# Kernel optimization log

Measured on AMD Instinct MI355X. Metric: run time of the kernel, lower is better.

Reference implementation:

```python
import jax, jax.numpy as jnp
import numpy as np

N, E, D = 50000, 600000, 128


def gcn_conv(x, edge_index, edge_weight, W, b, num_nodes):
    # PyG GCNConv (add_self_loops=False): out = D^{-1/2} A D^{-1/2} (x W) + b
    row, col = edge_index[0], edge_index[1]  # source, target
    deg = jax.ops.segment_sum(edge_weight, col, num_segments=num_nodes)  # [N]
    dis = jnp.where(deg > 0, jax.lax.rsqrt(jnp.where(deg > 0, deg, 1.0)), 0.0)
    norm = dis[row] * edge_weight * dis[col]  # [E]
    xl = x @ W  # [N, out]
    msg = xl[row] * norm[:, None]  # [E, out] gather + scale
    out = jax.ops.segment_sum(msg, col, num_segments=num_nodes)  # scatter-add
    return out + b


def setup_inputs() -> dict:
    key = jax.random.key(0)
    ks = jax.random.split(key, 7)
    x = jax.random.normal(ks[0], (N, D), dtype=jnp.float32)
    adj = jax.random.randint(ks[1], (2, E), 0, N, dtype=jnp.int64)
    edge_weights = jax.random.uniform(ks[2], (E,), dtype=jnp.float32)
    s = 1.0 / np.sqrt(D)
    W1 = jax.random.uniform(ks[3], (D, D), jnp.float32, -s, s)
    b1 = jnp.zeros((D,), jnp.float32)
    W2 = jax.random.uniform(ks[4], (D, D), jnp.float32, -s, s)
    b2 = jnp.zeros((D,), jnp.float32)
    return {"x": x, "adj": adj, "edge_weights": edge_weights,
            "W1": W1, "b1": b1, "W2": W2, "b2": b2}


def reference(x, adj, edge_weights, W1, b1, W2, b2):
    res = x
    h = gcn_conv(x, adj, edge_weights, W1, b1, N)
    h = jax.nn.relu(h)  # dropout is identity in eval mode
    h = gcn_conv(h, adj, edge_weights, W2, b2, N)
    h = jax.nn.relu(h)
    return h + res
```

## Files before the change

kernel.cpp:

```cpp
#include <hip/hip_runtime.h>
#include <hip/hip_bf16.h>

#define FEAT 128
#define CAP 64

typedef __attribute__((ext_vector_type(8))) short bf16x8;
typedef __attribute__((ext_vector_type(4))) float f32x4;

__device__ __forceinline__ short f2bf(float f) {
    __hip_bfloat16 h = __float2bfloat16(f);
    return *reinterpret_cast<short*>(&h);
}

__global__ __launch_bounds__(256) void k_prep(const float* __restrict__ W1,
                                              const float* __restrict__ W2,
                                              unsigned short* __restrict__ WT1,
                                              unsigned short* __restrict__ WT2,
                                              int* __restrict__ cur, int Nn) {
    const int tid = blockIdx.x * 256 + threadIdx.x;
    if (tid < FEAT * FEAT) {
        const int k = tid >> 7, n = tid & 127;
        WT1[n * FEAT + k] = (unsigned short)f2bf(W1[tid]);
        WT2[n * FEAT + k] = (unsigned short)f2bf(W2[tid]);
    }
    if (tid < Nn) cur[tid] = 0;
}

template <bool BF16IN>
__device__ __forceinline__ void gemm_tile(const void* __restrict__ Xv,
                                          const unsigned short* __restrict__ WT,
                                          unsigned short* __restrict__ Y,
                                          int Nn, int blk, int t) {
    const int rowBase = blk * 64;
    const int w = t >> 6;
    const int lane = t & 63;
    const int m = lane & 15;
    const int quad = lane >> 4;
    const int ar = rowBase + w * 16 + m;

    f32x4 acc[8] = {};
#pragma unroll
    for (int ks = 0; ks < 4; ++ks) {
        const int k0 = ks * 32 + quad * 8;
        bf16x8 a = {0, 0, 0, 0, 0, 0, 0, 0};
        if (ar < Nn) {
            if (BF16IN) {
                a = *(const bf16x8*)((const unsigned short*)Xv + (size_t)ar * FEAT + k0);
            } else {
                const float* xp = (const float*)Xv + (size_t)ar * FEAT + k0;
                const float4 v0 = *(const float4*)xp;
                const float4 v1 = *(const float4*)(xp + 4);
                a[0] = f2bf(v0.x); a[1] = f2bf(v0.y); a[2] = f2bf(v0.z); a[3] = f2bf(v0.w);
                a[4] = f2bf(v1.x); a[5] = f2bf(v1.y); a[6] = f2bf(v1.z); a[7] = f2bf(v1.w);
            }
        }
#pragma unroll
        for (int nt = 0; nt < 8; ++nt) {
            bf16x8 b = *(const bf16x8*)(WT + (size_t)(nt * 16 + m) * FEAT + k0);
            acc[nt] = __builtin_amdgcn_mfma_f32_16x16x32_bf16(a, b, acc[nt], 0, 0, 0);
        }
    }

#pragma unroll
    for (int nt = 0; nt < 8; ++nt) {
#pragma unroll
        for (int r4 = 0; r4 < 4; ++r4) {
            int gr = rowBase + w * 16 + quad * 4 + r4;
            if (gr < Nn)
                Y[(size_t)gr * FEAT + nt * 16 + m] = (unsigned short)f2bf(acc[nt][r4]);
        }
    }
}

__device__ __forceinline__ void fill_body(const int* __restrict__ row,
                                          const int* __restrict__ col,
                                          const float* __restrict__ ew,
                                          int* __restrict__ cur,
                                          unsigned long long* __restrict__ bucket,
                                          int E, int blk, int t) {
    int e = blk * 256 + t;
    if (e >= E) return;
    int c = col[e];
    int slot = atomicAdd(&cur[c], 1);
    if (slot < CAP) {
        unsigned long long v = (unsigned long long)(unsigned int)row[e] |
                               ((unsigned long long)__float_as_uint(ew[e]) << 32);
        bucket[(size_t)c * CAP + slot] = v;
    }
}

__global__ __launch_bounds__(256) void k_fused_gemm1_fill(
        const float* __restrict__ x, const unsigned short* __restrict__ WT1,
        unsigned short* __restrict__ xl, int Nn,
        const int* __restrict__ row, const int* __restrict__ col,
        const float* __restrict__ ew, int* __restrict__ cur,
        unsigned long long* __restrict__ bucket, int E, int gG) {
    if ((int)blockIdx.x < gG)
        gemm_tile<false>((const void*)x, WT1, xl, Nn, blockIdx.x, threadIdx.x);
    else
        fill_body(row, col, ew, cur, bucket, E, blockIdx.x - gG, threadIdx.x);
}

__global__ __launch_bounds__(256) void k_gemm2(const unsigned short* __restrict__ h1b,
                                               const unsigned short* __restrict__ WT2,
                                               unsigned short* __restrict__ xl, int Nn) {
    gemm_tile<true>((const void*)h1b, WT2, xl, Nn, blockIdx.x, threadIdx.x);
}

__global__ __launch_bounds__(256) void k_deg_dis(const int* __restrict__ cur,
                                                 const unsigned long long* __restrict__ bucket,
                                                 float* __restrict__ dis, int Nn) {
    const int n = (blockIdx.x * 256 + threadIdx.x) >> 6;
    const int lane = threadIdx.x & 63;
    if (n >= Nn) return;
    const int cnt = min(cur[n], CAP);
    float v = 0.0f;
    if (lane < cnt) {
        unsigned long long b = bucket[(size_t)n * CAP + lane];
        v = __uint_as_float((unsigned int)(b >> 32));
    }
#pragma unroll
    for (int m = 1; m < 64; m <<= 1) v += __shfl_xor(v, m, 64);
    if (lane == 0) dis[n] = (v > 0.0f) ? rsqrtf(v) : 0.0f;
}

template <int MODE>
__global__ __launch_bounds__(256) void k_gather(const int* __restrict__ cur,
                                                const unsigned long long* __restrict__ bucket,
                                                const float* __restrict__ dis,
                                                const unsigned int* __restrict__ XL2,
                                                const float* __restrict__ bias,
                                                const float* __restrict__ xres,
                                                void* __restrict__ OUTv, int Nn) {
    const int n = (blockIdx.x * 256 + threadIdx.x) >> 6;
    const int lane = threadIdx.x & 63;
    if (n >= Nn) return;
    const int cnt = min(cur[n], CAP);
    const float dn = dis[n];

    const uint2 be = ((const uint2*)(bucket + (size_t)n * CAP))[lane];
    const int   srcv = (int)be.x;
    float wv = 0.0f;
    if (lane < cnt) wv = __uint_as_float(be.y) * dis[be.x];

    float ax = 0.0f, ay = 0.0f;
    int e = 0;
    for (; e + 8 <= cnt; e += 8) {
        int s[8];
        float w[8];
        unsigned int p[8];
#pragma unroll
        for (int j = 0; j < 8; ++j) {
            s[j] = __shfl(srcv, e + j, 64);
            w[j] = __shfl(wv, e + j, 64);
        }
#pragma unroll
        for (int j = 0; j < 8; ++j) p[j] = XL2[(size_t)s[j] * (FEAT / 2) + lane];
#pragma unroll
        for (int j = 0; j < 8; ++j) {
            ax += __uint_as_float(p[j] << 16) * w[j];
            ay += __uint_as_float(p[j] & 0xffff0000u) * w[j];
        }
    }
    for (; e + 4 <= cnt; e += 4) {
        int s[4];
        float w[4];
        unsigned int p[4];
#pragma unroll
        for (int j = 0; j < 4; ++j) {
            s[j] = __shfl(srcv, e + j, 64);
            w[j] = __shfl(wv, e + j, 64);
        }
#pragma unroll
        for (int j = 0; j < 4; ++j) p[j] = XL2[(size_t)s[j] * (FEAT / 2) + lane];
#pragma unroll
        for (int j = 0; j < 4; ++j) {
            ax += __uint_as_float(p[j] << 16) * w[j];
            ay += __uint_as_float(p[j] & 0xffff0000u) * w[j];
        }
    }
    for (; e < cnt; ++e) {
        const int s = __shfl(srcv, e, 64);
        const float w = __shfl(wv, e, 64);
        const unsigned int p = XL2[(size_t)s * (FEAT / 2) + lane];
        ax += __uint_as_float(p << 16) * w;
        ay += __uint_as_float(p & 0xffff0000u) * w;
    }
    ax = fmaxf(ax * dn + bias[lane * 2], 0.0f);
    ay = fmaxf(ay * dn + bias[lane * 2 + 1], 0.0f);
    if (MODE == 0) {
        unsigned int r = ((unsigned int)(unsigned short)f2bf(ay) << 16) |
                         (unsigned int)(unsigned short)f2bf(ax);
        ((unsigned int*)OUTv)[(size_t)n * (FEAT / 2) + lane] = r;
    } else {
        const size_t o = (size_t)n * FEAT + lane * 2;
        ax += xres[o];
        ay += xres[o + 1];
        *(float2*)((float*)OUTv + o) = make_float2(ax, ay);
    }
}

extern "C" void kernel_launch(void* const* d_in, const int* in_sizes, int n_in,
                              void* d_out, int out_size, void* d_ws, size_t ws_size,
                              hipStream_t stream) {
    const float* x   = (const float*)d_in[0];
    const int*   adj = (const int*)d_in[1];
    const float* ew  = (const float*)d_in[2];
    const float* W1  = (const float*)d_in[3];
    const float* b1  = (const float*)d_in[4];
    const float* W2  = (const float*)d_in[5];
    const float* b2  = (const float*)d_in[6];

    const int Nn = in_sizes[0] / FEAT;
    const int E  = in_sizes[2];
    const int* row = adj;
    const int* col = adj + E;

    char* ws = (char*)d_ws;
    auto carve = [&](size_t bytes) {
        char* p = ws;
        ws += (bytes + 255) & ~(size_t)255;
        return p;
    };
    int*                cur    = (int*)carve((size_t)Nn * 4);
    float*              dis    = (float*)carve((size_t)Nn * 4);
    unsigned short*     WT1    = (unsigned short*)carve((size_t)FEAT * FEAT * 2);
    unsigned short*     WT2    = (unsigned short*)carve((size_t)FEAT * FEAT * 2);
    unsigned long long* bucket = (unsigned long long*)carve((size_t)Nn * CAP * 8);
    unsigned short*     xl     = (unsigned short*)carve((size_t)Nn * FEAT * 2);

    unsigned short* h1b = (unsigned short*)d_out;

    const int TB = 256;
    const int gE = (E + TB - 1) / TB;
    const int gG = (Nn + 63) / 64;
    const int gW = (Nn + 3) / 4;
    const int gP = (max(Nn, FEAT * FEAT) + TB - 1) / TB;

    k_prep<<<gP, TB, 0, stream>>>(W1, W2, WT1, WT2, cur, Nn);
    k_fused_gemm1_fill<<<gG + gE, TB, 0, stream>>>(x, WT1, xl, Nn,
                                                   row, col, ew, cur, bucket, E, gG);
    k_deg_dis<<<gW, TB, 0, stream>>>(cur, bucket, dis, Nn);

    k_gather<0><<<gW, TB, 0, stream>>>(cur, bucket, dis, (const unsigned int*)xl,
                                       b1, nullptr, (void*)h1b, Nn);

    k_gemm2<<<gG, TB, 0, stream>>>(h1b, WT2, xl, Nn);
    k_gather<1><<<gW, TB, 0, stream>>>(cur, bucket, dis, (const unsigned int*)xl,
                                       b2, x, d_out, Nn);
}
```

Before: 212.6 us.

## Fuse all stages into one persistent kernel with grid barriers

Replaces the six separate launches (prep, gemm1+fill, degree, gather1, gemm2, gather2) with a single persistent kernel of 1024 blocks that loops over work with grid-stride loops. Stages are separated by a software grid barrier built on an atomic counter. This removes per-launch overhead and inter-kernel gaps. In exchange it depends on all 1024 blocks being co-resident, or the barrier deadlocks, and it loses the per-stage grid sizing, so GEMM1 runs on only 256 blocks while the edge fill gets the rest.

```diff
diff --git a/kernel.cpp b/kernel.cpp
--- a/kernel.cpp
+++ b/kernel.cpp
@@ -3,6 +3,9 @@
 
 #define FEAT 128
 #define CAP 64
+#define NBLK 1024
+#define NTHR 256
+#define GEMM_BLKS 256
 
 typedef __attribute__((ext_vector_type(8))) short bf16x8;
 typedef __attribute__((ext_vector_type(4))) float f32x4;
@@ -12,26 +15,23 @@
     return *reinterpret_cast<short*>(&h);
 }
 
-__global__ __launch_bounds__(256) void k_prep(const float* __restrict__ W1,
-                                              const float* __restrict__ W2,
-                                              unsigned short* __restrict__ WT1,
-                                              unsigned short* __restrict__ WT2,
-                                              int* __restrict__ cur, int Nn) {
-    const int tid = blockIdx.x * 256 + threadIdx.x;
-    if (tid < FEAT * FEAT) {
-        const int k = tid >> 7, n = tid & 127;
-        WT1[n * FEAT + k] = (unsigned short)f2bf(W1[tid]);
-        WT2[n * FEAT + k] = (unsigned short)f2bf(W2[tid]);
-    }
-    if (tid < Nn) cur[tid] = 0;
+__device__ __forceinline__ void grid_barrier(int* __restrict__ bar, int target) {
+    __syncthreads();
+    if (threadIdx.x == 0) {
+        __threadfence();
+        atomicAdd(bar, 1);
+        while (atomicAdd(bar, 0) < target) {}
+        __threadfence();
+    }
+    __syncthreads();
 }
 
 template <bool BF16IN>
 __device__ __forceinline__ void gemm_tile(const void* __restrict__ Xv,
                                           const unsigned short* __restrict__ WT,
                                           unsigned short* __restrict__ Y,
-                                          int Nn, int blk, int t) {
-    const int rowBase = blk * 64;
+                                          int Nn, int tile, int t) {
+    const int rowBase = tile * 64;
     const int w = t >> 6;
     const int lane = t & 63;
     const int m = lane & 15;
@@ -60,7 +60,6 @@
             acc[nt] = __builtin_amdgcn_mfma_f32_16x16x32_bf16(a, b, acc[nt], 0, 0, 0);
         }
     }
-
 #pragma unroll
     for (int nt = 0; nt < 8; ++nt) {
 #pragma unroll
@@ -72,74 +71,20 @@
     }
 }
 
-__device__ __forceinline__ void fill_body(const int* __restrict__ row,
-                                          const int* __restrict__ col,
-                                          const float* __restrict__ ew,
-                                          int* __restrict__ cur,
-                                          unsigned long long* __restrict__ bucket,
-                                          int E, int blk, int t) {
-    int e = blk * 256 + t;
-    if (e >= E) return;
-    int c = col[e];
-    int slot = atomicAdd(&cur[c], 1);
-    if (slot < CAP) {
-        unsigned long long v = (unsigned long long)(unsigned int)row[e] |
-                               ((unsigned long long)__float_as_uint(ew[e]) << 32);
-        bucket[(size_t)c * CAP + slot] = v;
-    }
-}
-
-__global__ __launch_bounds__(256) void k_fused_gemm1_fill(
-        const float* __restrict__ x, const unsigned short* __restrict__ WT1,
-        unsigned short* __restrict__ xl, int Nn,
-        const int* __restrict__ row, const int* __restrict__ col,
-        const float* __restrict__ ew, int* __restrict__ cur,
-        unsigned long long* __restrict__ bucket, int E, int gG) {
-    if ((int)blockIdx.x < gG)
-        gemm_tile<false>((const void*)x, WT1, xl, Nn, blockIdx.x, threadIdx.x);
-    else
-        fill_body(row, col, ew, cur, bucket, E, blockIdx.x - gG, threadIdx.x);
-}
-
-__global__ __launch_bounds__(256) void k_gemm2(const unsigned short* __restrict__ h1b,
-                                               const unsigned short* __restrict__ WT2,
-                                               unsigned short* __restrict__ xl, int Nn) {
-    gemm_tile<true>((const void*)h1b, WT2, xl, Nn, blockIdx.x, threadIdx.x);
-}
-
-__global__ __launch_bounds__(256) void k_deg_dis(const int* __restrict__ cur,
-                                                 const unsigned long long* __restrict__ bucket,
-                                                 float* __restrict__ dis, int Nn) {
-    const int n = (blockIdx.x * 256 + threadIdx.x) >> 6;
-    const int lane = threadIdx.x & 63;
-    if (n >= Nn) return;
-    const int cnt = min(cur[n], CAP);
-    float v = 0.0f;
-    if (lane < cnt) {
-        unsigned long long b = bucket[(size_t)n * CAP + lane];
-        v = __uint_as_float((unsigned int)(b >> 32));
-    }
-#pragma unroll
-    for (int m = 1; m < 64; m <<= 1) v += __shfl_xor(v, m, 64);
-    if (lane == 0) dis[n] = (v > 0.0f) ? rsqrtf(v) : 0.0f;
-}
-
 template <int MODE>
-__global__ __launch_bounds__(256) void k_gather(const int* __restrict__ cur,
-                                                const unsigned long long* __restrict__ bucket,
-                                                const float* __restrict__ dis,
-                                                const unsigned int* __restrict__ XL2,
-                                                const float* __restrict__ bias,
-                                                const float* __restrict__ xres,
-                                                void* __restrict__ OUTv, int Nn) {
-    const int n = (blockIdx.x * 256 + threadIdx.x) >> 6;
-    const int lane = threadIdx.x & 63;
-    if (n >= Nn) return;
+__device__ __forceinline__ void gather_node(int n, int lane,
+                                            const int* __restrict__ cur,
+                                            const unsigned long long* __restrict__ bucket,
+                                            const float* __restrict__ dis,
+                                            const unsigned int* __restrict__ XL2,
+                                            const float* __restrict__ bias,
+                                            const float* __restrict__ xres,
+                                            void* __restrict__ OUTv) {
     const int cnt = min(cur[n], CAP);
     const float dn = dis[n];
 
     const uint2 be = ((const uint2*)(bucket + (size_t)n * CAP))[lane];
-    const int   srcv = (int)be.x;
+    const int srcv = (int)be.x;
     float wv = 0.0f;
     if (lane < cnt) wv = __uint_as_float(be.y) * dis[be.x];
 
@@ -200,6 +145,77 @@
     }
 }
 
+__global__ __launch_bounds__(NTHR, 4) void k_all(
+        const float* __restrict__ x, const int* __restrict__ adj,
+        const float* __restrict__ ew,
+        const float* __restrict__ W1, const float* __restrict__ b1,
+        const float* __restrict__ W2, const float* __restrict__ b2,
+        int* __restrict__ bar,
+        int* __restrict__ cur, float* __restrict__ dis,
+        unsigned short* __restrict__ WT1, unsigned short* __restrict__ WT2,
+        unsigned long long* __restrict__ bucket, unsigned short* __restrict__ xl,
+        void* __restrict__ dout, int Nn, int E) {
+    const int t = threadIdx.x;
+    const int b = blockIdx.x;
+    const int gid = b * NTHR + t;
+    const int gsz = NBLK * NTHR;
+    const int lane = t & 63;
+    const int waveId = gid >> 6;
+    const int nWaves = gsz >> 6;
+    const int* row = adj;
+    const int* col = adj + E;
+    const int nTiles = (Nn + 63) >> 6;
+
+    for (int i = gid; i < FEAT * FEAT; i += gsz) {
+        const int k = i >> 7, n = i & 127;
+        WT1[n * FEAT + k] = (unsigned short)f2bf(W1[i]);
+        WT2[n * FEAT + k] = (unsigned short)f2bf(W2[i]);
+    }
+    for (int i = gid; i < Nn; i += gsz) cur[i] = 0;
+    grid_barrier(bar, NBLK * 1);
+
+    if (b < GEMM_BLKS) {
+        for (int tile = b; tile < nTiles; tile += GEMM_BLKS)
+            gemm_tile<false>((const void*)x, WT1, xl, Nn, tile, t);
+    } else {
+        const int fgid = (b - GEMM_BLKS) * NTHR + t;
+        const int fsz = (NBLK - GEMM_BLKS) * NTHR;
+        for (int e = fgid; e < E; e += fsz) {
+            const int c = col[e];
+            const int slot = atomicAdd(&cur[c], 1);
+            if (slot < CAP)
+                bucket[(size_t)c * CAP + slot] =
+                    (unsigned long long)(unsigned int)row[e] |
+                    ((unsigned long long)__float_as_uint(ew[e]) << 32);
+        }
+    }
+    grid_barrier(bar, NBLK * 2);
+
+    for (int n = waveId; n < Nn; n += nWaves) {
+        const int cnt = min(cur[n], CAP);
+        float v = 0.0f;
+        if (lane < cnt)
+            v = __uint_as_float((unsigned int)(bucket[(size_t)n * CAP + lane] >> 32));
+#pragma unroll
+        for (int m = 1; m < 64; m <<= 1) v += __shfl_xor(v, m, 64);
+        if (lane == 0) dis[n] = (v > 0.0f) ? rsqrtf(v) : 0.0f;
+    }
+    grid_barrier(bar, NBLK * 3);
+
+    for (int n = waveId; n < Nn; n += nWaves)
+        gather_node<0>(n, lane, cur, bucket, dis, (const unsigned int*)xl, b1,
+                       nullptr, dout);
+    grid_barrier(bar, NBLK * 4);
+
+    for (int tile = b; tile < nTiles; tile += NBLK)
+        gemm_tile<true>((const void*)dout, WT2, xl, Nn, tile, t);
+    grid_barrier(bar, NBLK * 5);
+
+    for (int n = waveId; n < Nn; n += nWaves)
+        gather_node<1>(n, lane, cur, bucket, dis, (const unsigned int*)xl, b2,
+                       x, dout);
+}
+
 extern "C" void kernel_launch(void* const* d_in, const int* in_sizes, int n_in,
                               void* d_out, int out_size, void* d_ws, size_t ws_size,
                               hipStream_t stream) {
@@ -211,10 +227,8 @@
     const float* W2  = (const float*)d_in[5];
     const float* b2  = (const float*)d_in[6];
 
-    const int Nn = in_sizes[0] / FEAT;
-    const int E  = in_sizes[2];
-    const int* row = adj;
-    const int* col = adj + E;
+    int Nn = in_sizes[0] / FEAT;
+    int E  = in_sizes[2];
 
     char* ws = (char*)d_ws;
     auto carve = [&](size_t bytes) {
@@ -222,6 +236,7 @@
         ws += (bytes + 255) & ~(size_t)255;
         return p;
     };
+    int*                bar    = (int*)carve(256);
     int*                cur    = (int*)carve((size_t)Nn * 4);
     float*              dis    = (float*)carve((size_t)Nn * 4);
     unsigned short*     WT1    = (unsigned short*)carve((size_t)FEAT * FEAT * 2);
@@ -229,23 +244,9 @@
     unsigned long long* bucket = (unsigned long long*)carve((size_t)Nn * CAP * 8);
     unsigned short*     xl     = (unsigned short*)carve((size_t)Nn * FEAT * 2);
 
-    unsigned short* h1b = (unsigned short*)d_out;
-
-    const int TB = 256;
-    const int gE = (E + TB - 1) / TB;
-    const int gG = (Nn + 63) / 64;
-    const int gW = (Nn + 3) / 4;
-    const int gP = (max(Nn, FEAT * FEAT) + TB - 1) / TB;
-
-    k_prep<<<gP, TB, 0, stream>>>(W1, W2, WT1, WT2, cur, Nn);
-    k_fused_gemm1_fill<<<gG + gE, TB, 0, stream>>>(x, WT1, xl, Nn,
-                                                   row, col, ew, cur, bucket, E, gG);
-    k_deg_dis<<<gW, TB, 0, stream>>>(cur, bucket, dis, Nn);
-
-    k_gather<0><<<gW, TB, 0, stream>>>(cur, bucket, dis, (const unsigned int*)xl,
-                                       b1, nullptr, (void*)h1b, Nn);
-
-    k_gemm2<<<gG, TB, 0, stream>>>(h1b, WT2, xl, Nn);
-    k_gather<1><<<gW, TB, 0, stream>>>(cur, bucket, dis, (const unsigned int*)xl,
-                                       b2, x, d_out, Nn);
-}
+    hipMemsetAsync(bar, 0, 4, stream);
+
+    k_all<<<NBLK, NTHR, 0, stream>>>(x, adj, ew, W1, b1, W2, b2, bar,
+                                     cur, dis, WT1, WT2, bucket, xl,
+                                     d_out, Nn, E);
+}
```

After: 836.3 us. +293.3%, slower.
